# Performance work log

Hardware: AMD Instinct MI355X
Metric: run time of the kernel (lower is better)

The kernel has to match this reference:

```python
import jax, jax.numpy as jnp
import numpy as np

N_NODES = 100000


def gcn_conv(h_in, W, b, src, dst, ew, n_nodes):
    """PyG GCNConv: x' = D^{-1/2} (A + I) D^{-1/2} (x W) + b, with edge weights."""
    h = h_in @ W  # [N, F_out]
    loop = jnp.arange(n_nodes, dtype=src.dtype)
    row = jnp.concatenate([src, loop])            # sources (j)
    col = jnp.concatenate([dst, loop])            # targets (i)
    w = jnp.concatenate([ew, jnp.ones((n_nodes,), dtype=ew.dtype)])
    deg = jax.ops.segment_sum(w, col, num_segments=n_nodes)  # weighted in-degree incl. self-loops
    dinv = jnp.where(deg > 0, jax.lax.rsqrt(deg), 0.0)
    norm = dinv[row] * w * dinv[col]              # [E+N]
    msg = h[row] * norm[:, None]                  # gather + scale, [E+N, F_out]
    out = jax.ops.segment_sum(msg, col, num_segments=n_nodes)  # scatter to targets
    return out + b


def setup_inputs() -> dict:
    key = jax.random.key(0)
    k = jax.random.split(key, 6)
    N, E, F_in, F_hid = N_NODES, 3200000, 128, 64
    x = jax.random.normal(k[0], (N, F_in), dtype=jnp.float32)
    edge_index = jax.random.randint(k[1], (2, E), 0, N, dtype=jnp.int64)
    edge_weight = jax.random.uniform(k[2], (E,), dtype=jnp.float32)
    W1 = jax.random.normal(k[3], (F_in, F_hid), dtype=jnp.float32) * 0.1
    b1 = jnp.zeros((F_hid,), dtype=jnp.float32)
    W2 = jax.random.normal(k[4], (F_hid, 1), dtype=jnp.float32) * 0.1
    b2 = jnp.zeros((1,), dtype=jnp.float32)
    return {"x": x, "edge_index": edge_index, "edge_weight": edge_weight,
            "W1": W1, "b1": b1, "W2": W2, "b2": b2}


def reference(x, edge_index, edge_weight, W1, b1, W2, b2):
    n_nodes = x.shape[0]
    src, dst = edge_index[0], edge_index[1]
    h = jax.nn.relu(gcn_conv(x, W1, b1, src, dst, edge_weight, n_nodes))
    h = gcn_conv(h, W2, b2, src, dst, edge_weight, n_nodes)  # [N, 1]
    score = jax.nn.sigmoid(h)[:, 0]
    # degree-weighted scoring (original edges, no self-loops), scatter onto source
    deg_weighted = jax.ops.segment_sum(edge_weight, src, num_segments=n_nodes)
    deg_norm = deg_weighted / jnp.max(deg_weighted)
    return score * (1.0 + deg_norm)
```

## Files before the change

kernel.cpp:

```cpp
#include <hip/hip_runtime.h>
#include <hip/hip_fp16.h>
#include <math.h>

#define F_IN 128
#define F_HID 64
#define NWG 128
#define PT 1024
#define BSH 7
#define BSZ 128
#define BSHS 10
#define BSZS 1024
#define SEGCAP 6144

typedef float f32x2 __attribute__((ext_vector_type(2)));
typedef float f32x4 __attribute__((ext_vector_type(4)));
typedef __bf16 bf16x8 __attribute__((ext_vector_type(8)));

__device__ __forceinline__ unsigned char f32_to_fp8(float v) {
  unsigned r = __builtin_amdgcn_cvt_pk_fp8_f32(v, v, 0, false);
  return (unsigned char)(r & 0xFFu);
}

__device__ __forceinline__ __bf16 f32_bf16(float f) {
  unsigned u = __float_as_uint(f);
  unsigned r = (u + 0x7FFFu + ((u >> 16) & 1u)) >> 16;
  return __builtin_bit_cast(__bf16, (unsigned short)r);
}

__device__ __forceinline__ int2 nt_i2(const int2* p) {
  long long v = __builtin_nontemporal_load((const long long*)p);
  return make_int2((int)(v & 0xFFFFFFFFll), (int)(v >> 32));
}

__global__ void k_count(const int* __restrict__ src, const int* __restrict__ dst,
                        int* __restrict__ cntAll, int NBD, int NBS, int E) {
  extern __shared__ int sh[];
  int* hD = sh;
  int* hS = sh + NBD;
  int tid = threadIdx.x, w = blockIdx.x;
  for (int k = tid; k < NBD + NBS; k += PT) sh[k] = 0;
  __syncthreads();
  int C = (E + NWG - 1) / NWG;
  int e0 = w * C, e1 = min(E, e0 + C);
  for (int e = e0 + tid; e < e1; e += PT) {
    atomicAdd(&hD[dst[e] >> BSH], 1);
    atomicAdd(&hS[src[e] >> BSHS], 1);
  }
  __syncthreads();
  for (int b = tid; b < NBD; b += PT) cntAll[b * NWG + w] = hD[b];
  for (int b = tid; b < NBS; b += PT) cntAll[(NBD + b) * NWG + w] = hS[b];
}

__global__ void k_scanA(int* __restrict__ data, int* __restrict__ partials, int TOT) {
  __shared__ int lds[1024];
  int tid = threadIdx.x;
  int g = blockIdx.x * 1024 + tid;
  int v = (g < TOT) ? data[g] : 0;
  lds[tid] = v; __syncthreads();
  for (int o = 1; o < 1024; o <<= 1) {
    int t = (tid >= o) ? lds[tid - o] : 0;
    __syncthreads();
    lds[tid] += t;
    __syncthreads();
  }
  if (g < TOT) data[g] = lds[tid] - v;
  if (tid == 1023) partials[blockIdx.x] = lds[1023];
}

__global__ void k_scanB(int* partials, int nb, unsigned* maxbits) {
  __shared__ int lds[1024];
  int tid = threadIdx.x;
  if (tid == 0) *maxbits = 0u;
  int v = (tid < nb) ? partials[tid] : 0;
  lds[tid] = v; __syncthreads();
  for (int o = 1; o < 1024; o <<= 1) {
    int t = (tid >= o) ? lds[tid - o] : 0;
    __syncthreads();
    lds[tid] += t;
    __syncthreads();
  }
  if (tid < nb) partials[tid] = lds[tid] - v;
}

__global__ void k_scanC(int* __restrict__ data, const int* __restrict__ partials, int TOT) {
  int g = blockIdx.x * 1024 + threadIdx.x;
  if (g < TOT) data[g] += partials[g >> 10];
}

__global__ void k_part(const int* __restrict__ src, const int* __restrict__ dst,
                       const float* __restrict__ ew, const int* __restrict__ baseAll,
                       int2* __restrict__ gD, unsigned* __restrict__ gS,
                       int NBD, int NBS, int E) {
  extern __shared__ int sh[];
  int* cD = sh;
  int* cS = sh + NBD;
  int tid = threadIdx.x, w = blockIdx.x;
  for (int b = tid; b < NBD; b += PT) cD[b] = baseAll[b * NWG + w];
  for (int b = tid; b < NBS; b += PT) cS[b] = baseAll[(NBD + b) * NWG + w] - E;
  __syncthreads();
  int C = (E + NWG - 1) / NWG;
  int e0 = w * C, e1 = min(E, e0 + C);
  for (int e = e0 + tid; e < e1; e += PT) {
    int s = src[e], d = dst[e];
    float wv = ew[e];
    int pD = atomicAdd(&cD[d >> BSH], 1);
    gD[pD] = make_int2(s | ((d & (BSZ - 1)) << 24), __float_as_int(wv));
    int pS = atomicAdd(&cS[s >> BSHS], 1);
    gS[pS] = ((unsigned)(s & (BSZS - 1)) << 16) | (unsigned)__half_as_ushort(__float2half(wv));
  }
}

__global__ void k_csr(int2* __restrict__ gD, const int* __restrict__ baseAll,
                      int* __restrict__ off, float* __restrict__ dinv,
                      int NBD, int N, int E) {
  __shared__ int2 seg[SEGCAP];
  __shared__ int hist[BSZ];
  __shared__ int curs[BSZ];
  __shared__ float degf[BSZ];
  int tid = threadIdx.x, b = blockIdx.x;
  int bstart = baseAll[b * NWG];
  int bend = (b + 1 < NBD) ? baseAll[(b + 1) * NWG] : E;
  int cnt = bend - bstart;
  for (int k = tid; k < cnt; k += 256) seg[k] = gD[bstart + k];
  if (tid < BSZ) { hist[tid] = 0; degf[tid] = 0.f; }
  __syncthreads();
  for (int k = tid; k < cnt; k += 256) {
    int dl = (unsigned)seg[k].x >> 24;
    atomicAdd(&hist[dl], 1);
    atomicAdd(&degf[dl], __int_as_float(seg[k].y));
  }
  __syncthreads();
  int v = (tid < BSZ) ? hist[tid] : 0;
  for (int o = 1; o < BSZ; o <<= 1) {
    int t = (tid < BSZ && tid >= o) ? hist[tid - o] : 0;
    __syncthreads();
    if (tid < BSZ) hist[tid] += t;
    __syncthreads();
  }
  if (tid < BSZ) {
    int excl = hist[tid] - v;
    curs[tid] = excl;
    int node = b * BSZ + tid;
    if (node < N) {
      off[node] = bstart + excl;
      dinv[node] = rsqrtf(1.0f + degf[tid]);
    }
  }
  if (b == NBD - 1 && tid == 0) off[N] = E;
  __syncthreads();
  for (int k = tid; k < cnt; k += 256) {
    int2 ev = seg[k];
    int dl = (unsigned)ev.x >> 24;
    int slot = atomicAdd(&curs[dl], 1);
    gD[bstart + slot] = make_int2(ev.x & 0xFFFFFF, ev.y);
  }
}

__global__ void k_dw(const unsigned* __restrict__ gS, const int* __restrict__ baseAll,
                     float* __restrict__ dw, unsigned* maxbits,
                     int NBD, int NBS, int N, int E) {
  __shared__ float acc[BSZS];
  int tid = threadIdx.x, b = blockIdx.x;
  int bstart = baseAll[(NBD + b) * NWG] - E;
  int bend = (b + 1 < NBS) ? baseAll[(NBD + b + 1) * NWG] - E : E;
  acc[tid] = 0.f;
  __syncthreads();
  for (int k = bstart + tid; k < bend; k += BSZS) {
    unsigned p = gS[k];
    atomicAdd(&acc[p >> 16], __half2float(__ushort_as_half((unsigned short)(p & 0xFFFFu))));
  }
  __syncthreads();
  float m = 0.f;
  int node = b * BSZS + tid;
  if (node < N) { dw[node] = acc[tid]; m = acc[tid]; }
  for (int mm = 32; mm; mm >>= 1) m = fmaxf(m, __shfl_xor(m, mm, 64));
  if ((tid & 63) == 0) atomicMax(maxbits, __float_as_uint(m));
}

__global__ void k_gemm1(const float* __restrict__ x, const float* __restrict__ W1,
                        const float* __restrict__ dinv, unsigned char* __restrict__ g0, int N) {
  int lane = threadIdx.x & 63;
  int wid = (blockIdx.x * blockDim.x + threadIdx.x) >> 6;
  int nw = (gridDim.x * blockDim.x) >> 6;
  int l16 = lane & 15, lh = lane >> 4;
  bf16x8 bfrag[4][4];
#pragma unroll
  for (int cb = 0; cb < 4; ++cb)
#pragma unroll
    for (int kf = 0; kf < 4; ++kf)
#pragma unroll
      for (int i = 0; i < 8; ++i) {
        int k = kf * 32 + lh * 8 + i;
        bfrag[cb][kf][i] = f32_bf16(W1[k * F_HID + cb * 16 + l16]);
      }
  int ntiles = (N + 15) >> 4;
  for (int t = wid; t < ntiles; t += nw) {
    int rowbase = t << 4;
    int row = min(rowbase + l16, N - 1);
    bf16x8 afrag[4];
#pragma unroll
    for (int kf = 0; kf < 4; ++kf) {
      const f32x4* xp = (const f32x4*)(x + (size_t)row * F_IN + kf * 32 + lh * 8);
      f32x4 v0 = xp[0], v1 = xp[1];
#pragma unroll
      for (int i = 0; i < 4; ++i) afrag[kf][i] = f32_bf16(v0[i]);
#pragma unroll
      for (int i = 0; i < 4; ++i) afrag[kf][4 + i] = f32_bf16(v1[i]);
    }
    f32x4 acc[4] = {{0.f,0.f,0.f,0.f},{0.f,0.f,0.f,0.f},{0.f,0.f,0.f,0.f},{0.f,0.f,0.f,0.f}};
#pragma unroll
    for (int cb = 0; cb < 4; ++cb)
#pragma unroll
      for (int kf = 0; kf < 4; ++kf)
        acc[cb] = __builtin_amdgcn_mfma_f32_16x16x32_bf16(afrag[kf], bfrag[cb][kf], acc[cb], 0, 0, 0);
    if (rowbase + 16 <= N) {
      f32x4 dv = *(const f32x4*)(dinv + rowbase + lh * 4);
#pragma unroll
      for (int cb = 0; cb < 4; ++cb)
#pragma unroll
        for (int r = 0; r < 4; ++r) {
          int rr = rowbase + lh * 4 + r;
          g0[(size_t)rr * F_HID + cb * 16 + l16] = f32_to_fp8(acc[cb][r] * dv[r]);
        }
    } else {
#pragma unroll
      for (int cb = 0; cb < 4; ++cb)
#pragma unroll
        for (int r = 0; r < 4; ++r) {
          int rr = rowbase + lh * 4 + r;
          if (rr < N)
            g0[(size_t)rr * F_HID + cb * 16 + l16] = f32_to_fp8(acc[cb][r] * dinv[rr]);
        }
    }
  }
}

__global__ void k_agg1(const unsigned char* __restrict__ g0, const float* __restrict__ dinv,
                       const int* __restrict__ off, const int2* __restrict__ csr,
                       const float* __restrict__ b1, const float* __restrict__ W2,
                       float* __restrict__ u, int N) {
  int lane = threadIdx.x & 63;
  int grp = lane >> 3;
  int l8  = lane & 7;
  int i = (blockIdx.x * blockDim.x + threadIdx.x) >> 6;
  if (i >= N) return;
  const uint2* g0v = (const uint2*)g0;
  float acc[8] = {0.f, 0.f, 0.f, 0.f, 0.f, 0.f, 0.f, 0.f};
  if (grp == 0) {
    uint2 rv = g0v[(size_t)i * 8 + l8];
    f32x2 c0 = __builtin_amdgcn_cvt_pk_f32_fp8(rv.x, false);
    f32x2 c1 = __builtin_amdgcn_cvt_pk_f32_fp8(rv.x, true);
    f32x2 c2 = __builtin_amdgcn_cvt_pk_f32_fp8(rv.y, false);
    f32x2 c3 = __builtin_amdgcn_cvt_pk_f32_fp8(rv.y, true);
    acc[0] += c0.x; acc[1] += c0.y; acc[2] += c1.x; acc[3] += c1.y;
    acc[4] += c2.x; acc[5] += c2.y; acc[6] += c3.x; acc[7] += c3.y;
  }
  int p0 = off[i], p1 = off[i + 1];
  for (int p = p0; p < p1; p += 64) {
    int m = min(p1 - p, 64);
    int2 ed = make_int2(0, 0);
    if (lane < m) ed = nt_i2(&csr[p + lane]);
#pragma unroll
    for (int jj = 0; jj < 8; ++jj) {
      int j = jj * 8 + grp;
      int s = __shfl(ed.x, j, 64);
      float w = __int_as_float(__shfl(ed.y, j, 64));
      if (j < m) {
        uint2 rv = g0v[(size_t)s * 8 + l8];
        f32x2 c0 = __builtin_amdgcn_cvt_pk_f32_fp8(rv.x, false);
        f32x2 c1 = __builtin_amdgcn_cvt_pk_f32_fp8(rv.x, true);
        f32x2 c2 = __builtin_amdgcn_cvt_pk_f32_fp8(rv.y, false);
        f32x2 c3 = __builtin_amdgcn_cvt_pk_f32_fp8(rv.y, true);
        acc[0] = fmaf(w, c0.x, acc[0]); acc[1] = fmaf(w, c0.y, acc[1]);
        acc[2] = fmaf(w, c1.x, acc[2]); acc[3] = fmaf(w, c1.y, acc[3]);
        acc[4] = fmaf(w, c2.x, acc[4]); acc[5] = fmaf(w, c2.y, acc[5]);
        acc[6] = fmaf(w, c3.x, acc[6]); acc[7] = fmaf(w, c3.y, acc[7]);
      }
    }
  }
#pragma unroll
  for (int k = 0; k < 8; ++k) {
    acc[k] += __shfl_xor(acc[k], 8, 64);
    acc[k] += __shfl_xor(acc[k], 16, 64);
    acc[k] += __shfl_xor(acc[k], 32, 64);
  }
  float di = dinv[i];
  float pdt = 0.f;
#pragma unroll
  for (int k = 0; k < 8; ++k) {
    int f = l8 * 8 + k;
    float h = fmaxf(di * acc[k] + b1[f], 0.f);
    pdt = fmaf(h, W2[f], pdt);
  }
  pdt += __shfl_xor(pdt, 1, 64);
  pdt += __shfl_xor(pdt, 2, 64);
  pdt += __shfl_xor(pdt, 4, 64);
  if (lane == 0) u[i] = di * pdt;
}

__global__ void k_agg2_final(const float* __restrict__ u, const float* __restrict__ dinv,
                             const int* __restrict__ off, const int2* __restrict__ csr,
                             const float* __restrict__ b2, const float* __restrict__ dw,
                             const unsigned* __restrict__ maxbits,
                             float* __restrict__ out, int N) {
  int lane32 = threadIdx.x & 31;
  int i = blockIdx.x * 8 + (threadIdx.x >> 5);
  if (i >= N) return;
  float acc = (lane32 == 0) ? u[i] : 0.f;
  int p0 = off[i], p1 = off[i + 1];
  for (int p = p0 + lane32; p < p1; p += 32) {
    int2 ed = csr[p];
    acc = fmaf(__int_as_float(ed.y), u[ed.x], acc);
  }
  for (int mm = 16; mm; mm >>= 1) acc += __shfl_xor(acc, mm, 64);
  if (lane32 == 0) {
    float md = __uint_as_float(*maxbits);
    float z = dinv[i] * acc + b2[0];
    float sc = 1.0f / (1.0f + expf(-z));
    out[i] = sc * (1.0f + dw[i] / md);
  }
}

extern "C" void kernel_launch(void* const* d_in, const int* in_sizes, int n_in,
                              void* d_out, int out_size, void* d_ws, size_t ws_size,
                              hipStream_t stream) {
  const float* x  = (const float*)d_in[0];
  const int*   ei = (const int*)d_in[1];
  const float* ew = (const float*)d_in[2];
  const float* W1 = (const float*)d_in[3];
  const float* b1 = (const float*)d_in[4];
  const float* W2 = (const float*)d_in[5];
  const float* b2 = (const float*)d_in[6];
  float* out = (float*)d_out;

  int N = out_size;
  int E = in_sizes[2];
  const int* src = ei;
  const int* dst = ei + E;

  int NBD = (N + BSZ - 1) >> BSH;
  int NBS = (N + BSZS - 1) >> BSHS;
  int TOT = (NBD + NBS) * NWG;
  int SB = (TOT + 1023) >> 10;
  size_t shmem = (size_t)(NBD + NBS) * sizeof(int);

  char* w8 = (char*)d_ws;
  int2*     gD      = (int2*)w8;
  unsigned* gS      = (unsigned*)(gD + E);
  int*      cntAll  = (int*)(gS + E);
  int*      partials= cntAll + TOT;
  int*      off     = partials + 1024;
  float*    dinv    = (float*)(off + N + 1);
  float*    dw      = dinv + N;
  float*    u       = dw + N;
  unsigned* maxbits = (unsigned*)(u + N);
  unsigned char* g0 = (unsigned char*)(maxbits + 4);

  k_count<<<NWG, PT, shmem, stream>>>(src, dst, cntAll, NBD, NBS, E);
  k_scanA<<<SB, 1024, 0, stream>>>(cntAll, partials, TOT);
  k_scanB<<<1, 1024, 0, stream>>>(partials, SB, maxbits);
  k_scanC<<<SB, 1024, 0, stream>>>(cntAll, partials, TOT);
  k_part<<<NWG, PT, shmem, stream>>>(src, dst, ew, cntAll, gD, gS, NBD, NBS, E);
  k_csr<<<NBD, 256, 0, stream>>>(gD, cntAll, off, dinv, NBD, N, E);
  k_dw<<<NBS, BSZS, 0, stream>>>(gS, cntAll, dw, maxbits, NBD, NBS, N, E);
  k_gemm1<<<256, 256, 0, stream>>>(x, W1, dinv, g0, N);
  k_agg1<<<(N * 64 + 255) / 256, 256, 0, stream>>>(g0, dinv, off, gD, b1, W2, u, N);
  k_agg2_final<<<(N + 7) / 8, 256, 0, stream>>>(u, dinv, off, gD, b2, dw, maxbits, out, N);
}
```

Measured before the change: 299.0 us.

## Pad per-workgroup partition runs to 8-edge alignment and double partition workgroups

Doubles the number of partition workgroups and rounds each destination-bucket run up to a multiple of 8 slots, filling the padding with sentinel entries that the CSR build filters out while staging into LDS. Per-node degrees are stored separately so the aggregation kernels no longer read off[i+1]. Edge input reads use nontemporal loads, and the layer-1 accumulation uses packed two-wide FMAs. The intent is aligned partition writes and more parallelism in count and partition, at the cost of extra workspace, padding writes and an atomic compaction step in k_csr.

```diff
diff --git a/kernel.cpp b/kernel.cpp
--- a/kernel.cpp
+++ b/kernel.cpp
@@ -4,7 +4,7 @@
 
 #define F_IN 128
 #define F_HID 64
-#define NWG 128
+#define NWG 256
 #define PT 1024
 #define BSH 7
 #define BSZ 128
@@ -43,27 +43,29 @@
   int C = (E + NWG - 1) / NWG;
   int e0 = w * C, e1 = min(E, e0 + C);
   for (int e = e0 + tid; e < e1; e += PT) {
-    atomicAdd(&hD[dst[e] >> BSH], 1);
-    atomicAdd(&hS[src[e] >> BSHS], 1);
+    atomicAdd(&hD[__builtin_nontemporal_load(&dst[e]) >> BSH], 1);
+    atomicAdd(&hS[__builtin_nontemporal_load(&src[e]) >> BSHS], 1);
   }
   __syncthreads();
   for (int b = tid; b < NBD; b += PT) cntAll[b * NWG + w] = hD[b];
   for (int b = tid; b < NBS; b += PT) cntAll[(NBD + b) * NWG + w] = hS[b];
 }
 
-__global__ void k_scanA(int* __restrict__ data, int* __restrict__ partials, int TOT) {
+__global__ void k_scanA(int* __restrict__ data, int* __restrict__ partials,
+                        int TOT, int DSTREG) {
   __shared__ int lds[1024];
   int tid = threadIdx.x;
   int g = blockIdx.x * 1024 + tid;
   int v = (g < TOT) ? data[g] : 0;
-  lds[tid] = v; __syncthreads();
+  int pv = (g < DSTREG) ? ((v + 7) & ~7) : v;
+  lds[tid] = pv; __syncthreads();
   for (int o = 1; o < 1024; o <<= 1) {
     int t = (tid >= o) ? lds[tid - o] : 0;
     __syncthreads();
     lds[tid] += t;
     __syncthreads();
   }
-  if (g < TOT) data[g] = lds[tid] - v;
+  if (g < TOT) data[g] = lds[tid] - pv;
   if (tid == 1023) partials[blockIdx.x] = lds[1023];
 }
 
@@ -95,35 +97,52 @@
   int* cD = sh;
   int* cS = sh + NBD;
   int tid = threadIdx.x, w = blockIdx.x;
+  int PADTOT = baseAll[NBD * NWG];
   for (int b = tid; b < NBD; b += PT) cD[b] = baseAll[b * NWG + w];
-  for (int b = tid; b < NBS; b += PT) cS[b] = baseAll[(NBD + b) * NWG + w] - E;
+  for (int b = tid; b < NBS; b += PT) cS[b] = baseAll[(NBD + b) * NWG + w] - PADTOT;
   __syncthreads();
   int C = (E + NWG - 1) / NWG;
   int e0 = w * C, e1 = min(E, e0 + C);
   for (int e = e0 + tid; e < e1; e += PT) {
-    int s = src[e], d = dst[e];
-    float wv = ew[e];
+    int s = __builtin_nontemporal_load(&src[e]);
+    int d = __builtin_nontemporal_load(&dst[e]);
+    float wv = __builtin_nontemporal_load(&ew[e]);
     int pD = atomicAdd(&cD[d >> BSH], 1);
     gD[pD] = make_int2(s | ((d & (BSZ - 1)) << 24), __float_as_int(wv));
     int pS = atomicAdd(&cS[s >> BSHS], 1);
     gS[pS] = ((unsigned)(s & (BSZS - 1)) << 16) | (unsigned)__half_as_ushort(__float2half(wv));
   }
+  __syncthreads();
+  for (int b = tid; b < NBD; b += PT) {
+    int end = cD[b];
+    int padEnd = (end + 7) & ~7;
+    for (int p = end; p < padEnd; ++p) gD[p] = make_int2((int)0xFF000000u, 0);
+  }
 }
 
 __global__ void k_csr(int2* __restrict__ gD, const int* __restrict__ baseAll,
-                      int* __restrict__ off, float* __restrict__ dinv,
-                      int NBD, int N, int E) {
+                      int* __restrict__ off, int* __restrict__ degN,
+                      float* __restrict__ dinv, int NBD, int N) {
   __shared__ int2 seg[SEGCAP];
   __shared__ int hist[BSZ];
   __shared__ int curs[BSZ];
   __shared__ float degf[BSZ];
+  __shared__ int nstage;
   int tid = threadIdx.x, b = blockIdx.x;
   int bstart = baseAll[b * NWG];
-  int bend = (b + 1 < NBD) ? baseAll[(b + 1) * NWG] : E;
-  int cnt = bend - bstart;
-  for (int k = tid; k < cnt; k += 256) seg[k] = gD[bstart + k];
+  int bend = baseAll[(b + 1) * NWG];
+  if (tid == 0) nstage = 0;
   if (tid < BSZ) { hist[tid] = 0; degf[tid] = 0.f; }
   __syncthreads();
+  for (int k = bstart + tid; k < bend; k += 256) {
+    int2 ev = gD[k];
+    if (((unsigned)ev.x >> 24) < 128u) {
+      int sl = atomicAdd(&nstage, 1);
+      seg[sl] = ev;
+    }
+  }
+  __syncthreads();
+  int cnt = nstage;
   for (int k = tid; k < cnt; k += 256) {
     int dl = (unsigned)seg[k].x >> 24;
     atomicAdd(&hist[dl], 1);
@@ -143,10 +162,10 @@
     int node = b * BSZ + tid;
     if (node < N) {
       off[node] = bstart + excl;
+      degN[node] = v;
       dinv[node] = rsqrtf(1.0f + degf[tid]);
     }
   }
-  if (b == NBD - 1 && tid == 0) off[N] = E;
   __syncthreads();
   for (int k = tid; k < cnt; k += 256) {
     int2 ev = seg[k];
@@ -161,8 +180,9 @@
                      int NBD, int NBS, int N, int E) {
   __shared__ float acc[BSZS];
   int tid = threadIdx.x, b = blockIdx.x;
-  int bstart = baseAll[(NBD + b) * NWG] - E;
-  int bend = (b + 1 < NBS) ? baseAll[(NBD + b + 1) * NWG] - E : E;
+  int PADTOT = baseAll[NBD * NWG];
+  int bstart = baseAll[(NBD + b) * NWG] - PADTOT;
+  int bend = (b + 1 < NBS) ? baseAll[(NBD + b + 1) * NWG] - PADTOT : E;
   acc[tid] = 0.f;
   __syncthreads();
   for (int k = bstart + tid; k < bend; k += BSZS) {
@@ -236,7 +256,8 @@
 }
 
 __global__ void k_agg1(const unsigned char* __restrict__ g0, const float* __restrict__ dinv,
-                       const int* __restrict__ off, const int2* __restrict__ csr,
+                       const int* __restrict__ off, const int* __restrict__ degN,
+                       const int2* __restrict__ csr,
                        const float* __restrict__ b1, const float* __restrict__ W2,
                        float* __restrict__ u, int N) {
   int lane = threadIdx.x & 63;
@@ -245,17 +266,15 @@
   int i = (blockIdx.x * blockDim.x + threadIdx.x) >> 6;
   if (i >= N) return;
   const uint2* g0v = (const uint2*)g0;
-  float acc[8] = {0.f, 0.f, 0.f, 0.f, 0.f, 0.f, 0.f, 0.f};
+  f32x2 acc2[4] = {{0.f,0.f},{0.f,0.f},{0.f,0.f},{0.f,0.f}};
   if (grp == 0) {
     uint2 rv = g0v[(size_t)i * 8 + l8];
-    f32x2 c0 = __builtin_amdgcn_cvt_pk_f32_fp8(rv.x, false);
-    f32x2 c1 = __builtin_amdgcn_cvt_pk_f32_fp8(rv.x, true);
-    f32x2 c2 = __builtin_amdgcn_cvt_pk_f32_fp8(rv.y, false);
-    f32x2 c3 = __builtin_amdgcn_cvt_pk_f32_fp8(rv.y, true);
-    acc[0] += c0.x; acc[1] += c0.y; acc[2] += c1.x; acc[3] += c1.y;
-    acc[4] += c2.x; acc[5] += c2.y; acc[6] += c3.x; acc[7] += c3.y;
-  }
-  int p0 = off[i], p1 = off[i + 1];
+    acc2[0] += __builtin_amdgcn_cvt_pk_f32_fp8(rv.x, false);
+    acc2[1] += __builtin_amdgcn_cvt_pk_f32_fp8(rv.x, true);
+    acc2[2] += __builtin_amdgcn_cvt_pk_f32_fp8(rv.y, false);
+    acc2[3] += __builtin_amdgcn_cvt_pk_f32_fp8(rv.y, true);
+  }
+  int p0 = off[i], p1 = p0 + degN[i];
   for (int p = p0; p < p1; p += 64) {
     int m = min(p1 - p, 64);
     int2 ed = make_int2(0, 0);
@@ -267,17 +286,16 @@
       float w = __int_as_float(__shfl(ed.y, j, 64));
       if (j < m) {
         uint2 rv = g0v[(size_t)s * 8 + l8];
-        f32x2 c0 = __builtin_amdgcn_cvt_pk_f32_fp8(rv.x, false);
-        f32x2 c1 = __builtin_amdgcn_cvt_pk_f32_fp8(rv.x, true);
-        f32x2 c2 = __builtin_amdgcn_cvt_pk_f32_fp8(rv.y, false);
-        f32x2 c3 = __builtin_amdgcn_cvt_pk_f32_fp8(rv.y, true);
-        acc[0] = fmaf(w, c0.x, acc[0]); acc[1] = fmaf(w, c0.y, acc[1]);
-        acc[2] = fmaf(w, c1.x, acc[2]); acc[3] = fmaf(w, c1.y, acc[3]);
-        acc[4] = fmaf(w, c2.x, acc[4]); acc[5] = fmaf(w, c2.y, acc[5]);
-        acc[6] = fmaf(w, c3.x, acc[6]); acc[7] = fmaf(w, c3.y, acc[7]);
+        f32x2 w2; w2.x = w; w2.y = w;
+        acc2[0] = __builtin_elementwise_fma(__builtin_amdgcn_cvt_pk_f32_fp8(rv.x, false), w2, acc2[0]);
+        acc2[1] = __builtin_elementwise_fma(__builtin_amdgcn_cvt_pk_f32_fp8(rv.x, true),  w2, acc2[1]);
+        acc2[2] = __builtin_elementwise_fma(__builtin_amdgcn_cvt_pk_f32_fp8(rv.y, false), w2, acc2[2]);
+        acc2[3] = __builtin_elementwise_fma(__builtin_amdgcn_cvt_pk_f32_fp8(rv.y, true),  w2, acc2[3]);
       }
     }
   }
+  float acc[8] = {acc2[0].x, acc2[0].y, acc2[1].x, acc2[1].y,
+                  acc2[2].x, acc2[2].y, acc2[3].x, acc2[3].y};
 #pragma unroll
   for (int k = 0; k < 8; ++k) {
     acc[k] += __shfl_xor(acc[k], 8, 64);
@@ -299,7 +317,8 @@
 }
 
 __global__ void k_agg2_final(const float* __restrict__ u, const float* __restrict__ dinv,
-                             const int* __restrict__ off, const int2* __restrict__ csr,
+                             const int* __restrict__ off, const int* __restrict__ degN,
+                             const int2* __restrict__ csr,
                              const float* __restrict__ b2, const float* __restrict__ dw,
                              const unsigned* __restrict__ maxbits,
                              float* __restrict__ out, int N) {
@@ -307,7 +326,7 @@
   int i = blockIdx.x * 8 + (threadIdx.x >> 5);
   if (i >= N) return;
   float acc = (lane32 == 0) ? u[i] : 0.f;
-  int p0 = off[i], p1 = off[i + 1];
+  int p0 = off[i], p1 = p0 + degN[i];
   for (int p = p0 + lane32; p < p1; p += 32) {
     int2 ed = csr[p];
     acc = fmaf(__int_as_float(ed.y), u[ed.x], acc);
@@ -341,29 +360,32 @@
   int NBD = (N + BSZ - 1) >> BSH;
   int NBS = (N + BSZS - 1) >> BSHS;
   int TOT = (NBD + NBS) * NWG;
+  int DSTREG = NBD * NWG;
   int SB = (TOT + 1023) >> 10;
   size_t shmem = (size_t)(NBD + NBS) * sizeof(int);
+  size_t gDcap = (size_t)E + (size_t)7 * NBD * NWG + 1024;
 
   char* w8 = (char*)d_ws;
   int2*     gD      = (int2*)w8;
-  unsigned* gS      = (unsigned*)(gD + E);
+  unsigned* gS      = (unsigned*)(gD + gDcap);
   int*      cntAll  = (int*)(gS + E);
   int*      partials= cntAll + TOT;
   int*      off     = partials + 1024;
-  float*    dinv    = (float*)(off + N + 1);
+  int*      degN    = off + N;
+  float*    dinv    = (float*)(degN + N);
   float*    dw      = dinv + N;
   float*    u       = dw + N;
   unsigned* maxbits = (unsigned*)(u + N);
   unsigned char* g0 = (unsigned char*)(maxbits + 4);
 
   k_count<<<NWG, PT, shmem, stream>>>(src, dst, cntAll, NBD, NBS, E);
-  k_scanA<<<SB, 1024, 0, stream>>>(cntAll, partials, TOT);
+  k_scanA<<<SB, 1024, 0, stream>>>(cntAll, partials, TOT, DSTREG);
   k_scanB<<<1, 1024, 0, stream>>>(partials, SB, maxbits);
   k_scanC<<<SB, 1024, 0, stream>>>(cntAll, partials, TOT);
   k_part<<<NWG, PT, shmem, stream>>>(src, dst, ew, cntAll, gD, gS, NBD, NBS, E);
-  k_csr<<<NBD, 256, 0, stream>>>(gD, cntAll, off, dinv, NBD, N, E);
+  k_csr<<<NBD, 256, 0, stream>>>(gD, cntAll, off, degN, dinv, NBD, N);
   k_dw<<<NBS, BSZS, 0, stream>>>(gS, cntAll, dw, maxbits, NBD, NBS, N, E);
   k_gemm1<<<256, 256, 0, stream>>>(x, W1, dinv, g0, N);
-  k_agg1<<<(N * 64 + 255) / 256, 256, 0, stream>>>(g0, dinv, off, gD, b1, W2, u, N);
-  k_agg2_final<<<(N + 7) / 8, 256, 0, stream>>>(u, dinv, off, gD, b2, dw, maxbits, out, N);
-}
+  k_agg1<<<(N * 64 + 255) / 256, 256, 0, stream>>>(g0, dinv, off, degN, gD, b1, W2, u, N);
+  k_agg2_final<<<(N + 7) / 8, 256, 0, stream>>>(u, dinv, off, degN, gD, b2, dw, maxbits, out, N);
+}
```

Measured after the change: 337.4 us. 1.13x slower.
